# Performance work log

Hardware: AMD Instinct MI355X
Metric: run time of the kernel (lower is better)

## Reference

```python
import jax, jax.numpy as jnp
import numpy as np

NUM_FEAT = 1024
NUM_GROUP = 16
DIM_K = NUM_FEAT // NUM_GROUP  # 64
FEAT_DIM = 64
WAVE_LENGTH = 1000.0


def position_embedding(box, ctx_box):
    # box: (M,4), ctx_box: (N,4) corner encoding -> (M*N, 64)
    xmin, ymin, xmax, ymax = jnp.split(box, 4, axis=1)            # (M,1) each
    bw = xmax - xmin + 1.0
    bh = ymax - ymin + 1.0
    cx = 0.5 * (xmin + xmax)
    cy = 0.5 * (ymin + ymax)
    cxmin, cymin, cxmax, cymax = jnp.split(ctx_box, 4, axis=1)    # (N,1) each
    cbw = cxmax - cxmin + 1.0
    cbh = cymax - cymin + 1.0
    ccx = 0.5 * (cxmin + cxmax)
    ccy = 0.5 * (cymin + cymax)
    dx = jnp.log(jnp.clip(jnp.abs((cx - ccx.T) / bw), 1e-3))      # (M,N)
    dy = jnp.log(jnp.clip(jnp.abs((cy - ccy.T) / bh), 1e-3))
    dw = jnp.log(cbw.T / bw)
    dh = jnp.log(cbh.T / bh)
    pos = jnp.stack((dx, dy, dw, dh), axis=2)                     # (M,N,4)
    feat_range = jnp.arange(FEAT_DIM // 8, dtype=jnp.float32)     # (8,)
    dim_mat = jnp.power(jnp.float32(WAVE_LENGTH), (8.0 / FEAT_DIM) * feat_range)
    div = (100.0 * pos)[..., None] / dim_mat                      # (M,N,4,8)
    emb = jnp.concatenate((jnp.sin(div), jnp.cos(div)), axis=3)   # (M,N,4,16)
    M, N = pos.shape[0], pos.shape[1]
    return emb.reshape(M * N, FEAT_DIM)


def setup_inputs() -> dict:
    key = jax.random.key(0)
    ks = jax.random.split(key, 12)
    M, N = 512, 1024

    def make_boxes(k, n):
        k1, k2 = jax.random.split(k)
        xy = jax.random.uniform(k1, (n, 2), dtype=jnp.float32) * 800.0
        wh = jax.random.uniform(k2, (n, 2), dtype=jnp.float32) * 200.0 + 1.0
        return jnp.concatenate([xy, xy + wh], axis=1)             # valid corners

    return {
        "feat": jax.random.normal(ks[0], (M, NUM_FEAT), dtype=jnp.float32),
        "ctx_feat": jax.random.normal(ks[1], (N, NUM_FEAT), dtype=jnp.float32),
        "box": make_boxes(ks[2], M),
        "ctx_box": make_boxes(ks[3], N),
        # torch Linear stores weight as (out, in); apply as x @ W.T + b
        "w_fc_gt": jax.random.normal(ks[4], (NUM_FEAT, 1024), dtype=jnp.float32) * 0.01,
        "b_fc_gt": jnp.zeros((NUM_FEAT,), dtype=jnp.float32),
        "w_fc_ctx": jax.random.normal(ks[5], (NUM_FEAT, 1024), dtype=jnp.float32) * 0.01,
        "b_fc_ctx": jnp.zeros((NUM_FEAT,), dtype=jnp.float32),
        "w_pos_gt": jax.random.normal(ks[6], (NUM_GROUP, FEAT_DIM), dtype=jnp.float32) * 0.01,
        "b_pos_gt": jnp.zeros((NUM_GROUP,), dtype=jnp.float32),
        "w_pos_ctx": jax.random.normal(ks[7], (NUM_GROUP, FEAT_DIM), dtype=jnp.float32) * 0.01,
        "b_pos_ctx": jnp.zeros((NUM_GROUP,), dtype=jnp.float32),
        # grouped 1x1 conv (16384 -> 1024, groups=16): per-group weight (64 out, 1024 in)
        "w_conv": jax.random.normal(ks[8], (NUM_GROUP, DIM_K, NUM_FEAT), dtype=jnp.float32) * 0.02,
        "b_conv": jnp.zeros((NUM_FEAT,), dtype=jnp.float32),
    }


def reference(feat, ctx_feat, box, ctx_box,
              w_fc_gt, b_fc_gt, w_fc_ctx, b_fc_ctx,
              w_pos_gt, b_pos_gt, w_pos_ctx, b_pos_ctx,
              w_conv, b_conv):
    M, N = feat.shape[0], ctx_feat.shape[0]
    # positional bias per group: (M*N,64) -relu-> linear -> (G,M,N)
    pe_gt = jax.nn.relu(position_embedding(box, ctx_box))
    pos_gt = (pe_gt @ w_pos_gt.T + b_pos_gt).T.reshape(NUM_GROUP, M, N)
    pe_ctx = jax.nn.relu(position_embedding(ctx_box, box))
    pos_ctx = (pe_ctx @ w_pos_ctx.T + b_pos_ctx).T.reshape(NUM_GROUP, N, M)
    # grouped projections
    q = (feat @ w_fc_gt.T + b_fc_gt).reshape(M, NUM_GROUP, DIM_K)
    k = (ctx_feat @ w_fc_ctx.T + b_fc_ctx).reshape(N, NUM_GROUP, DIM_K)
    scores = jnp.einsum('mgd,ngd->gmn', q, k) / np.float32(np.sqrt(DIM_K))  # (G,M,N)
    # gt <- ctx attention with log-position bias
    w1 = jax.nn.softmax(jnp.log(jnp.clip(pos_gt, 1e-6)) + scores, axis=-1)  # (G,M,N)
    att1 = jnp.einsum('gmn,nc->mgc', w1, ctx_feat)                          # (M,G,1024)
    out_gt = jnp.einsum('mgc,goc->mgo', att1, w_conv).reshape(M, NUM_FEAT) + b_conv
    # ctx <- gt attention (note: original module reuses gt_ctx_linear_out here)
    w2 = jax.nn.softmax(jnp.log(jnp.clip(pos_ctx, 1e-6)) + scores.transpose(0, 2, 1), axis=-1)  # (G,N,M)
    att2 = jnp.einsum('gnm,mc->ngc', w2, feat)                              # (N,G,1024)
    out_ctx = jnp.einsum('ngc,goc->ngo', att2, w_conv).reshape(N, NUM_FEAT) + b_conv
    return out_gt, out_ctx
```

## Files before the change

kernel.cpp:

```cpp
#include <hip/hip_runtime.h>
#include <math.h>


typedef __attribute__((ext_vector_type(8))) short short8;
typedef __attribute__((ext_vector_type(4))) float floatx4;
typedef __attribute__((ext_vector_type(4))) _Float16 half4;
typedef __attribute__((ext_vector_type(4))) unsigned uint4v;

__device__ inline unsigned short f32_bf16_rne(float x) {
    union { float f; unsigned u; } v; v.f = x;
    unsigned u = v.u;
    return (unsigned short)((u + 0x7fffu + ((u >> 16) & 1u)) >> 16);
}

__device__ inline unsigned fbits(float x) {
    union { float f; unsigned u; } v; v.f = x; return v.u;
}
__device__ inline float bitsf(unsigned u) {
    union { unsigned u; float f; } v; v.u = u; return v.f;
}

__device__ __forceinline__ floatx4 mfma16(short8 a, short8 b, floatx4 c) {
    return __builtin_amdgcn_mfma_f32_16x16x32_bf16(a, b, c, 0, 0, 0);
}

__device__ __forceinline__ void gemm_tile_pack(
    const unsigned short* __restrict__ Ab, int lda,
    const unsigned short* __restrict__ Bb, int ldb, int K,
    unsigned short* __restrict__ out_base,
    const float* __restrict__ biasvec,
    unsigned short* As, unsigned short* Bs)
{
    const int tid = threadIdx.x;
    const int lr = tid >> 3;
    const int lk = (tid & 7) * 8;
    const int lane = tid & 63;
    const int wave = tid >> 6;
    const int qr = (wave >> 1) * 32;
    const int qc = (wave & 1) * 32;
    const int m = lane & 15;
    const int quad = lane >> 4;

    const unsigned short* Ap  = Ab + (long long)lr * lda + lk;
    const unsigned short* Ap2 = Ap + 32LL * lda;
    const unsigned short* Bp  = Bb + (long long)lr * ldb + lk;
    const unsigned short* Bp2 = Bp + 32LL * ldb;
    unsigned short* AsW  = As + lr * 72 + lk;
    unsigned short* AsW2 = As + (lr + 32) * 72 + lk;
    unsigned short* BsW  = Bs + lr * 72 + lk;
    unsigned short* BsW2 = Bs + (lr + 32) * 72 + lk;
    const unsigned short* a0p = As + (qr + m) * 72 + quad * 8;
    const unsigned short* b0p = Bs + (qc + m) * 72 + quad * 8;

    floatx4 acc00 = {0.f,0.f,0.f,0.f}, acc01 = {0.f,0.f,0.f,0.f};
    floatx4 acc10 = {0.f,0.f,0.f,0.f}, acc11 = {0.f,0.f,0.f,0.f};

    int4 pa0 = *(const int4*)Ap;
    int4 pa1 = *(const int4*)Ap2;
    int4 pb0 = *(const int4*)Bp;
    int4 pb1 = *(const int4*)Bp2;
    int4 qa0 = *(const int4*)(Ap + 64);
    int4 qa1 = *(const int4*)(Ap2 + 64);
    int4 qb0 = *(const int4*)(Bp + 64);
    int4 qb1 = *(const int4*)(Bp2 + 64);

    for (int k0 = 0; ; ) {
        __syncthreads();
        *(int4*)AsW  = pa0;
        *(int4*)AsW2 = pa1;
        *(int4*)BsW  = pb0;
        *(int4*)BsW2 = pb1;
        __syncthreads();
        pa0 = qa0; pa1 = qa1; pb0 = qb0; pb1 = qb1;
        const int kf = k0 + 128;
        if (kf < K) {
            qa0 = *(const int4*)(Ap + kf);
            qa1 = *(const int4*)(Ap2 + kf);
            qb0 = *(const int4*)(Bp + kf);
            qb1 = *(const int4*)(Bp2 + kf);
        }
        #pragma unroll
        for (int kk = 0; kk < 64; kk += 32) {
            short8 a0 = *(const short8*)(a0p + kk);
            short8 a1 = *(const short8*)(a0p + 16 * 72 + kk);
            short8 b0 = *(const short8*)(b0p + kk);
            short8 b1 = *(const short8*)(b0p + 16 * 72 + kk);
            acc00 = mfma16(a0, b0, acc00);
            acc01 = mfma16(a0, b1, acc01);
            acc10 = mfma16(a1, b0, acc10);
            acc11 = mfma16(a1, b1, acc11);
        }
        k0 += 64;
        if (k0 >= K) break;
    }

    float bias0 = 0.f, bias1 = 0.f;
    if (biasvec) { bias0 = biasvec[qc + m]; bias1 = biasvec[qc + 16 + m]; }

    __syncthreads();
    const floatx4 accs[2][2] = { {acc00, acc01}, {acc10, acc11} };
    #pragma unroll
    for (int i = 0; i < 2; ++i)
        #pragma unroll
        for (int r = 0; r < 4; ++r) {
            const int lrow = qr + i * 16 + quad * 4 + r;
            #pragma unroll
            for (int j = 0; j < 2; ++j) {
                const int lcol = qc + j * 16 + m;
                float val = accs[i][j][r] + (j ? bias1 : bias0);
                As[lrow * 72 + lcol] = f32_bf16_rne(val);
            }
        }
    __syncthreads();
    #pragma unroll
    for (int h = 0; h < 2; ++h) {
        const int f = h * 2048 + tid * 8;
        const int lanep = (f >> 3) & 63;
        const int part = (f >> 9) & 1;
        const int ploc = f >> 10;
        const int row = ploc * 16 + (lanep & 15);
        const int col = part * 32 + ((lanep >> 4) << 3);
        short8 v8 = *(const short8*)&As[row * 72 + col];
        *(short8*)(out_base + f) = v8;
    }
}

__global__ __launch_bounds__(256) void projvt_kernel(
    const unsigned short* __restrict__ in_bf, const unsigned short* __restrict__ wgt,
    const unsigned short* __restrict__ wctx,
    const float* __restrict__ bgt, const float* __restrict__ bctx,
    unsigned short* __restrict__ qk_pack,
    const unsigned short* __restrict__ wconv, unsigned short* __restrict__ vt_pack)
{
    __shared__ __align__(16) unsigned short As[64 * 72];
    __shared__ __align__(16) unsigned short Bs[64 * 72];
    if (blockIdx.z == 0) {
        const int bm = blockIdx.x * 64;
        const int g = blockIdx.y;
        const unsigned short* B = (bm < 512) ? wgt : wctx;
        const float* bias = (bm < 512) ? bgt : bctx;
        gemm_tile_pack(in_bf + (long long)bm * 1024, 1024,
                       B + (long long)g * 65536, 1024, 1024,
                       qk_pack + ((long long)g * 96 + blockIdx.x * 4) * 1024,
                       bias + g * 64, As, Bs);
    } else {
        const int cc = blockIdx.x;
        const int g = blockIdx.y;
        gemm_tile_pack(wconv + (long long)g * 65536, 1024,
                       in_bf + (long long)cc * 65536, 1024, 1024,
                       vt_pack + ((long long)g * 24 + cc) * 4096,
                       nullptr, As, Bs);
    }
}

__global__ __launch_bounds__(256) void prep_kernel(
    const float* __restrict__ box, const float* __restrict__ ctx_box,
    const float* __restrict__ w_gt, const float* __restrict__ b_gt,
    const float* __restrict__ w_ctx, const float* __restrict__ b_ctx,
    _Float16* __restrict__ bias_gt, _Float16* __restrict__ bias_ctx,
    const float* s0, unsigned short* d0, int n0,
    const float* s1, unsigned short* d1, int n1,
    const float* s2, unsigned short* d2, int n2,
    const float* s3, unsigned short* d3, int n3,
    const float* s4, unsigned short* d4, int n4)
{
    const int bx = blockIdx.x;
    if (bx >= 4096) {
        const int bc = bx - 4096;
        const int which = bc >> 10;
        const int xb = bc & 1023;
        const float* s; unsigned short* d; int n;
        switch (which) {
            case 0: s = s0; d = d0; n = n0; break;
            case 1: s = s1; d = d1; n = n1; break;
            case 2: s = s2; d = d2; n = n2; break;
            case 3: s = s3; d = d3; n = n3; break;
            default: s = s4; d = d4; n = n4; break;
        }
        int idx = (xb * 256 + threadIdx.x) * 4;
        if (idx < n) {
            float4 v = *(const float4*)(s + idx);
            ushort4 o;
            o.x = f32_bf16_rne(v.x); o.y = f32_bf16_rne(v.y);
            o.z = f32_bf16_rne(v.z); o.w = f32_bf16_rne(v.w);
            *(ushort4*)(d + idx) = o;
        }
        return;
    }

    const bool first = (bx < 2048);
    const long long blk = first ? bx : (bx - 2048);
    const float* boxA = first ? box : ctx_box;
    const float* boxB = first ? ctx_box : box;
    const float* w_pos = first ? w_gt : w_ctx;
    const float* b_pos = first ? b_gt : b_ctx;
    _Float16* out = first ? bias_gt : bias_ctx;
    const int shift = first ? 10 : 9;

    __shared__ __align__(16) unsigned short BsH[16 * 72];
    __shared__ __align__(16) unsigned short BsL[16 * 72];
    __shared__ float posL[4 * 68];
    __shared__ _Float16 stg[16 * 68];

    const int tid = threadIdx.x;

    {
        const int g = tid >> 4;
        const int d = (tid & 15) * 4;
        float4 wv = *(const float4*)(w_pos + g * 64 + d);
        unsigned u0 = fbits(wv.x), u1 = fbits(wv.y);
        unsigned u2 = fbits(wv.z), u3 = fbits(wv.w);
        unsigned r0 = fbits(wv.x - bitsf(u0 & 0xFFFF0000u));
        unsigned r1 = fbits(wv.y - bitsf(u1 & 0xFFFF0000u));
        unsigned r2 = fbits(wv.z - bitsf(u2 & 0xFFFF0000u));
        unsigned r3 = fbits(wv.w - bitsf(u3 & 0xFFFF0000u));
        uint2 hv, lv;
        hv.x = (u0 >> 16) | (u1 & 0xFFFF0000u);
        hv.y = (u2 >> 16) | (u3 & 0xFFFF0000u);
        lv.x = (r0 >> 16) | (r1 & 0xFFFF0000u);
        lv.y = (r2 >> 16) | (r3 & 0xFFFF0000u);
        *(uint2*)&BsH[g * 72 + d] = hv;
        *(uint2*)&BsL[g * 72 + d] = lv;
    }
    __syncthreads();

    const int lane = tid & 63;
    const int w = tid >> 6;
    const int m = lane & 15;
    const int quad = lane >> 4;
    const bool qlow = (quad < 2);
    const float phase = (quad & 1) ? 1.57079632679f : 0.0f;
    const float bpv = b_pos[m];

    const unsigned short* bpH = &BsH[m * 72 + quad * 8];
    const unsigned short* bpL = &BsL[m * 72 + quad * 8];
    short8 bH0 = *(const short8*)bpH;
    short8 bH1 = *(const short8*)(bpH + 32);
    short8 bL0 = *(const short8*)bpL;
    short8 bL1 = *(const short8*)(bpL + 32);

    const float w100[8] = {100.f, 42.169650342f, 17.782794100f, 7.498942093f,
                           3.162277660f, 1.333521432f, 0.562341325f, 0.237137371f};
    const long long pbase = blk * 256;

    for (int it = 0; it < 4; ++it) {
        const long long pb = pbase + it * 64;

        {
            const int pl = tid & 63;
            const int p = tid >> 6;
            const long long pair = pb + pl;
            const int i = (int)(pair >> shift);
            const int j = (int)(pair & ((1 << shift) - 1));
            float4 ba = *(const float4*)(boxA + i * 4);
            float4 bb = *(const float4*)(boxB + j * 4);
            float posv;
            if (p == 0) {
                float r = __builtin_amdgcn_rcpf(ba.z - ba.x + 1.f);
                posv = __logf(fmaxf(fabsf((0.5f*(ba.x+ba.z) - 0.5f*(bb.x+bb.z)) * r), 1e-3f));
            } else if (p == 1) {
                float r = __builtin_amdgcn_rcpf(ba.w - ba.y + 1.f);
                posv = __logf(fmaxf(fabsf((0.5f*(ba.y+ba.w) - 0.5f*(bb.y+bb.w)) * r), 1e-3f));
            } else if (p == 2) {
                float r = __builtin_amdgcn_rcpf(ba.z - ba.x + 1.f);
                posv = __logf((bb.z - bb.x + 1.f) * r);
            } else {
                float r = __builtin_amdgcn_rcpf(ba.w - ba.y + 1.f);
                posv = __logf((bb.w - bb.y + 1.f) * r);
            }
            posL[p * 68 + pl] = posv;
        }
        __syncthreads();

        const int plB = w * 16 + m;
        const float pos_lo = posL[(qlow ? 0 : 1) * 68 + plB];
        const float pos_hi = posL[(qlow ? 2 : 3) * 68 + plB];

        unsigned hp0[4], lp0[4], hp1[4], lp1[4];
        #pragma unroll
        for (int fi = 0; fi < 4; ++fi) {
            float x0 = fmaxf(__sinf(fmaf(w100[2*fi],     pos_lo, phase)), 0.f);
            float x1 = fmaxf(__sinf(fmaf(w100[2*fi + 1], pos_lo, phase)), 0.f);
            unsigned u0 = fbits(x0), u1 = fbits(x1);
            unsigned r0 = fbits(x0 - bitsf(u0 & 0xFFFF0000u));
            unsigned r1 = fbits(x1 - bitsf(u1 & 0xFFFF0000u));
            hp0[fi] = (u0 >> 16) | (u1 & 0xFFFF0000u);
            lp0[fi] = (r0 >> 16) | (r1 & 0xFFFF0000u);
            float y0 = fmaxf(__sinf(fmaf(w100[2*fi],     pos_hi, phase)), 0.f);
            float y1 = fmaxf(__sinf(fmaf(w100[2*fi + 1], pos_hi, phase)), 0.f);
            unsigned v0 = fbits(y0), v1 = fbits(y1);
            unsigned s0r = fbits(y0 - bitsf(v0 & 0xFFFF0000u));
            unsigned s1r = fbits(y1 - bitsf(v1 & 0xFFFF0000u));
            hp1[fi] = (v0 >> 16) | (v1 & 0xFFFF0000u);
            lp1[fi] = (s0r >> 16) | (s1r & 0xFFFF0000u);
        }
        union { uint4v u; short8 s; } cH0, cL0, cH1, cL1;
        cH0.u = (uint4v){hp0[0], hp0[1], hp0[2], hp0[3]};
        cL0.u = (uint4v){lp0[0], lp0[1], lp0[2], lp0[3]};
        cH1.u = (uint4v){hp1[0], hp1[1], hp1[2], hp1[3]};
        cL1.u = (uint4v){lp1[0], lp1[1], lp1[2], lp1[3]};

        floatx4 acc = {0.f, 0.f, 0.f, 0.f};
        acc = mfma16(cH0.s, bH0, acc);
        acc = mfma16(cH1.s, bH1, acc);
        acc = mfma16(cH0.s, bL0, acc);
        acc = mfma16(cH1.s, bL1, acc);
        acc = mfma16(cL0.s, bH0, acc);
        acc = mfma16(cL1.s, bH1, acc);

        #pragma unroll
        for (int r = 0; r < 4; ++r)
            stg[m * 68 + w * 16 + quad * 4 + r] =
                (_Float16)__logf(fmaxf(acc[r] + bpv, 1e-6f));
        __syncthreads();

        const int g2 = tid >> 4, c16 = tid & 15;
        *(half4*)(out + (long long)g2 * 524288 + pb + c16 * 4) =
            *(const half4*)&stg[g2 * 68 + c16 * 4];
    }
}

template <int NC>
__device__ __forceinline__ void attn_body(
    int g, int bx,
    const unsigned short* __restrict__ qk, int pA, int pB0,
    const _Float16* __restrict__ bias,
    const unsigned short* __restrict__ vt, int cc0,
    const float* __restrict__ b_conv, float* __restrict__ outp,
    unsigned short* wpack, float* redA, float* redB)
{
    constexpr int NCOL = NC * 64;
    constexpr int WS = NCOL + 8;
    constexpr int SHIFT = (NC == 16) ? 10 : 9;

    const int bm = bx * 16;
    const int tid = threadIdx.x;
    const int lane = tid & 63;
    const int w = tid >> 6;
    const int m = lane & 15;
    const int quad = lane >> 4;

    _Float16* bb = (_Float16*)wpack;
    {
        const _Float16* bsrc = bias + (long long)g * 524288 + (long long)bm * NCOL;
        #pragma unroll
        for (int i = 0; i < (16 * NCOL) / (256 * 8); ++i) {
            const int idx = (i * 256 + tid) * 8;
            const int row = idx >> SHIFT;
            const int col = idx & (NCOL - 1);
            *(int4*)(bb + row * WS + col) = *(const int4*)(bsrc + idx);
        }
    }

    const unsigned short* abase = qk + ((long long)(g * 96 + pA)) * 1024;
    short8 aq0 = *(const short8*)(abase + lane * 8);
    short8 aq1 = *(const short8*)(abase + 512 + lane * 8);

    const unsigned short* bptr = qk + ((long long)(g * 96 + pB0 + w)) * 1024 + lane * 8;
    short8 B0[2], B1[2];
    B0[0] = *(const short8*)bptr;
    B1[0] = *(const short8*)(bptr + 512);
    B0[1] = *(const short8*)(bptr + 4096);
    B1[1] = *(const short8*)(bptr + 4096 + 512);

    __syncthreads();

    const _Float16* brow = bb + (quad * 4) * WS + w * 16 + m;

    float v[NC][4];
    #pragma unroll
    for (int c = 0; c < NC; ++c) {
        float bv[4];
        #pragma unroll
        for (int r = 0; r < 4; ++r)
            bv[r] = (float)brow[r * WS + c * 64];
        floatx4 acc = {0.f, 0.f, 0.f, 0.f};
        acc = mfma16(aq0, B0[c & 1], acc);
        acc = mfma16(aq1, B1[c & 1], acc);
        if (c + 2 < NC) {
            const unsigned short* nb = bptr + (long long)(c + 2) * 4096;
            B0[c & 1] = *(const short8*)nb;
            B1[c & 1] = *(const short8*)(nb + 512);
        }
        #pragma unroll
        for (int r = 0; r < 4; ++r)
            v[c][r] = fmaf(0.125f, acc[r], bv[r]);
    }

    const unsigned short* vptr = vt + ((long long)(g * 24 + cc0)) * 4096
                               + w * 1024 + lane * 8;
    short8 V0[2], V1[2];
    V0[0] = *(const short8*)vptr;
    V1[0] = *(const short8*)(vptr + 512);
    V0[1] = *(const short8*)(vptr + 4096);
    V1[1] = *(const short8*)(vptr + 4096 + 512);

    float rmax[4];
    #pragma unroll
    for (int r = 0; r < 4; ++r) {
        float mx = v[0][r];
        #pragma unroll
        for (int c = 1; c < NC; ++c) mx = fmaxf(mx, v[c][r]);
        #pragma unroll
        for (int off = 1; off < 16; off <<= 1)
            mx = fmaxf(mx, __shfl_xor(mx, off, 64));
        rmax[r] = mx;
    }
    if (m == 0) {
        #pragma unroll
        for (int r = 0; r < 4; ++r) redA[w * 16 + quad * 4 + r] = rmax[r];
    }
    __syncthreads();
    #pragma unroll
    for (int r = 0; r < 4; ++r)
        rmax[r] = fmaxf(fmaxf(redA[quad*4+r], redA[16 + quad*4+r]),
                        fmaxf(redA[32 + quad*4+r], redA[48 + quad*4+r]));

    float rsum[4] = {0.f, 0.f, 0.f, 0.f};
    #pragma unroll
    for (int c = 0; c < NC; ++c)
        #pragma unroll
        for (int r = 0; r < 4; ++r) {
            v[c][r] = __expf(v[c][r] - rmax[r]);
            rsum[r] += v[c][r];
        }
    #pragma unroll
    for (int r = 0; r < 4; ++r)
        #pragma unroll
        for (int off = 1; off < 16; off <<= 1)
            rsum[r] += __shfl_xor(rsum[r], off, 64);
    if (m == 0) {
        #pragma unroll
        for (int r = 0; r < 4; ++r) redB[w * 16 + quad * 4 + r] = rsum[r];
    }
    __syncthreads();
    float rinv[4];
    #pragma unroll
    for (int r = 0; r < 4; ++r)
        rinv[r] = 1.f / (redB[quad*4+r] + redB[16 + quad*4+r] +
                         redB[32 + quad*4+r] + redB[48 + quad*4+r]);

    #pragma unroll
    for (int c = 0; c < NC; ++c)
        #pragma unroll
        for (int r = 0; r < 4; ++r)
            wpack[(quad * 4 + r) * WS + c * 64 + w * 16 + m] =
                f32_bf16_rne(v[c][r] * rinv[r]);

    __syncthreads();

    floatx4 oacc = {0.f, 0.f, 0.f, 0.f};
    const unsigned short* awp = wpack + m * WS + quad * 8;
    #pragma unroll
    for (int kc = 0; kc < NC; ++kc) {
        short8 a0 = *(const short8*)(awp + kc * 64);
        short8 a1 = *(const short8*)(awp + kc * 64 + 32);
        oacc = mfma16(a0, V0[kc & 1], oacc);
        oacc = mfma16(a1, V1[kc & 1], oacc);
        if (kc + 2 < NC) {
            const unsigned short* nv = vptr + (long long)(kc + 2) * 4096;
            V0[kc & 1] = *(const short8*)nv;
            V1[kc & 1] = *(const short8*)(nv + 512);
        }
    }

    const int o = w * 16 + m;
    const float bc = b_conv[g * 64 + o];
    __syncthreads();
    float* ot = (float*)wpack;
    #pragma unroll
    for (int r = 0; r < 4; ++r)
        ot[(quad * 4 + r) * 68 + o] = oacc[r] + bc;
    __syncthreads();
    const int orow = tid >> 4, oc4 = (tid & 15) * 4;
    float4 ov = *(const float4*)&ot[orow * 68 + oc4];
    *(float4*)(outp + (long long)(bm + orow) * 1024 + g * 64 + oc4) = ov;
}

__global__ __launch_bounds__(256) void attn_out_kernel(
    const unsigned short* __restrict__ qk_pack,
    const _Float16* __restrict__ bias_gt, const _Float16* __restrict__ bias_ctx,
    const unsigned short* __restrict__ vt_pack, const float* __restrict__ b_conv,
    float* __restrict__ out_gt, float* __restrict__ out_ctx)
{
    __shared__ __align__(16) unsigned short wpack[16 * 1032];
    __shared__ float redA[64], redB[64];

    const int bx = blockIdx.x;
    if (bx < 512) {
        const int rb = bx & 31;
        attn_body<16>(bx >> 5, rb, qk_pack, rb, 32,
                      bias_gt, vt_pack, 8, b_conv, out_gt,
                      wpack, redA, redB);
    } else {
        const int b2 = bx - 512;
        const int rb = b2 & 63;
        attn_body<8>(b2 >> 6, rb, qk_pack, 32 + rb, 0,
                     bias_ctx, vt_pack, 0, b_conv, out_ctx,
                     wpack, redA, redB);
    }
}

extern "C" void kernel_launch(void* const* d_in, const int* in_sizes, int n_in,
                              void* d_out, int out_size, void* d_ws, size_t ws_size,
                              hipStream_t stream)
{
    const float* feat     = (const float*)d_in[0];
    const float* ctx_feat = (const float*)d_in[1];
    const float* box      = (const float*)d_in[2];
    const float* ctx_box  = (const float*)d_in[3];
    const float* w_fc_gt  = (const float*)d_in[4];
    const float* b_fc_gt  = (const float*)d_in[5];
    const float* w_fc_ctx = (const float*)d_in[6];
    const float* b_fc_ctx = (const float*)d_in[7];
    const float* w_pos_gt = (const float*)d_in[8];
    const float* b_pos_gt = (const float*)d_in[9];
    const float* w_pos_ctx= (const float*)d_in[10];
    const float* b_pos_ctx= (const float*)d_in[11];
    const float* w_conv   = (const float*)d_in[12];
    const float* b_conv   = (const float*)d_in[13];

    float* ws = (float*)d_ws;
    unsigned short* in_bf   = (unsigned short*)ws;
    unsigned short* ctx_bf  = in_bf + 524288LL;
    unsigned short* qk_pack = in_bf + 1572864LL;
    _Float16* bias_gt  = (_Float16*)(ws + 1572864LL);
    _Float16* bias_ctx = (_Float16*)(ws + 5767168LL);
    unsigned short* wconv_bf = (unsigned short*)(ws + 9961472LL);
    unsigned short* vt_pack  = (unsigned short*)(ws + 10485760LL);
    unsigned short* wfcgt_bf = (unsigned short*)(ws + 11272192LL);
    unsigned short* wfcctx_bf= wfcgt_bf + 1048576LL;

    float* out_gt  = (float*)d_out;
    float* out_ctx = (float*)d_out + 524288LL;

    hipLaunchKernelGGL(prep_kernel, dim3(9216), dim3(256), 0, stream,
                       box, ctx_box, w_pos_gt, b_pos_gt, w_pos_ctx, b_pos_ctx,
                       bias_gt, bias_ctx,
                       feat, in_bf, 524288,
                       ctx_feat, ctx_bf, 1048576,
                       w_fc_gt, wfcgt_bf, 1048576,
                       w_fc_ctx, wfcctx_bf, 1048576,
                       w_conv, wconv_bf, 1048576);

    hipLaunchKernelGGL(projvt_kernel, dim3(24, 16, 2), dim3(256), 0, stream,
                       in_bf, wfcgt_bf, wfcctx_bf, b_fc_gt, b_fc_ctx, qk_pack,
                       wconv_bf, vt_pack);

    hipLaunchKernelGGL(attn_out_kernel, dim3(1536), dim3(256), 0, stream,
                       qk_pack, bias_gt, bias_ctx, vt_pack, b_conv, out_gt, out_ctx);
}
```

Measured before the change: 150.2 us.

## Split casts into own kernel and co-schedule projection GEMMs with position-bias blocks

Moves the fp32-to-bf16 casts into a separate first kernel. The position-embedding bias computation and the Q/K/V projection GEMM tiles now share one launch, with GEMM blocks interleaved every sixth block id, so the latency-bound GEMM tiles overlap with the transcendental-heavy bias work. Shared memory is unified into one buffer sized for the GEMM tiles, which may lower occupancy for the bias blocks.

```diff
diff --git a/kernel.cpp b/kernel.cpp
--- a/kernel.cpp
+++ b/kernel.cpp
@@ -125,71 +125,70 @@
     }
 }
 
-__global__ __launch_bounds__(256) void projvt_kernel(
+__global__ __launch_bounds__(256) void cast_kernel(
+    const float* __restrict__ s0, unsigned short* __restrict__ d0,
+    const float* __restrict__ s1, unsigned short* __restrict__ d1,
+    const float* __restrict__ s2, unsigned short* __restrict__ d2,
+    const float* __restrict__ s3, unsigned short* __restrict__ d3,
+    const float* __restrict__ s4, unsigned short* __restrict__ d4)
+{
+    int bc = blockIdx.x;
+    const float* s; unsigned short* d;
+    if (bc < 512)       { s = s0; d = d0; }
+    else if (bc < 1536) { s = s1; d = d1; bc -= 512; }
+    else if (bc < 2560) { s = s2; d = d2; bc -= 1536; }
+    else if (bc < 3584) { s = s3; d = d3; bc -= 2560; }
+    else                { s = s4; d = d4; bc -= 3584; }
+    const int idx = (bc * 256 + threadIdx.x) * 4;
+    float4 v = *(const float4*)(s + idx);
+    ushort4 o;
+    o.x = f32_bf16_rne(v.x); o.y = f32_bf16_rne(v.y);
+    o.z = f32_bf16_rne(v.z); o.w = f32_bf16_rne(v.w);
+    *(ushort4*)(d + idx) = o;
+}
+
+__global__ __launch_bounds__(256) void posproj_kernel(
+    const float* __restrict__ box, const float* __restrict__ ctx_box,
+    const float* __restrict__ w_gt, const float* __restrict__ b_gt,
+    const float* __restrict__ w_ctx, const float* __restrict__ b_ctx,
+    _Float16* __restrict__ bias_gt, _Float16* __restrict__ bias_ctx,
     const unsigned short* __restrict__ in_bf, const unsigned short* __restrict__ wgt,
     const unsigned short* __restrict__ wctx,
     const float* __restrict__ bgt, const float* __restrict__ bctx,
     unsigned short* __restrict__ qk_pack,
     const unsigned short* __restrict__ wconv, unsigned short* __restrict__ vt_pack)
 {
-    __shared__ __align__(16) unsigned short As[64 * 72];
-    __shared__ __align__(16) unsigned short Bs[64 * 72];
-    if (blockIdx.z == 0) {
-        const int bm = blockIdx.x * 64;
-        const int g = blockIdx.y;
-        const unsigned short* B = (bm < 512) ? wgt : wctx;
-        const float* bias = (bm < 512) ? bgt : bctx;
-        gemm_tile_pack(in_bf + (long long)bm * 1024, 1024,
-                       B + (long long)g * 65536, 1024, 1024,
-                       qk_pack + ((long long)g * 96 + blockIdx.x * 4) * 1024,
-                       bias + g * 64, As, Bs);
-    } else {
-        const int cc = blockIdx.x;
-        const int g = blockIdx.y;
-        gemm_tile_pack(wconv + (long long)g * 65536, 1024,
-                       in_bf + (long long)cc * 65536, 1024, 1024,
-                       vt_pack + ((long long)g * 24 + cc) * 4096,
-                       nullptr, As, Bs);
-    }
-}
-
-__global__ __launch_bounds__(256) void prep_kernel(
-    const float* __restrict__ box, const float* __restrict__ ctx_box,
-    const float* __restrict__ w_gt, const float* __restrict__ b_gt,
-    const float* __restrict__ w_ctx, const float* __restrict__ b_ctx,
-    _Float16* __restrict__ bias_gt, _Float16* __restrict__ bias_ctx,
-    const float* s0, unsigned short* d0, int n0,
-    const float* s1, unsigned short* d1, int n1,
-    const float* s2, unsigned short* d2, int n2,
-    const float* s3, unsigned short* d3, int n3,
-    const float* s4, unsigned short* d4, int n4)
-{
-    const int bx = blockIdx.x;
-    if (bx >= 4096) {
-        const int bc = bx - 4096;
-        const int which = bc >> 10;
-        const int xb = bc & 1023;
-        const float* s; unsigned short* d; int n;
-        switch (which) {
-            case 0: s = s0; d = d0; n = n0; break;
-            case 1: s = s1; d = d1; n = n1; break;
-            case 2: s = s2; d = d2; n = n2; break;
-            case 3: s = s3; d = d3; n = n3; break;
-            default: s = s4; d = d4; n = n4; break;
-        }
-        int idx = (xb * 256 + threadIdx.x) * 4;
-        if (idx < n) {
-            float4 v = *(const float4*)(s + idx);
-            ushort4 o;
-            o.x = f32_bf16_rne(v.x); o.y = f32_bf16_rne(v.y);
-            o.z = f32_bf16_rne(v.z); o.w = f32_bf16_rne(v.w);
-            *(ushort4*)(d + idx) = o;
+    __shared__ __align__(16) unsigned short smem[64 * 72 * 2];
+    const int i = blockIdx.x;
+
+    if (i < 4608 && (i % 6) == 0) {
+        const int gi = i / 6;
+        const int z = gi / 384;
+        const int rem = gi - z * 384;
+        const int g = rem / 24;
+        const int cc = rem - g * 24;
+        unsigned short* As = smem;
+        unsigned short* Bs = smem + 64 * 72;
+        if (z == 0) {
+            const int bm = cc * 64;
+            const unsigned short* B = (bm < 512) ? wgt : wctx;
+            const float* bias = (bm < 512) ? bgt : bctx;
+            gemm_tile_pack(in_bf + (long long)bm * 1024, 1024,
+                           B + (long long)g * 65536, 1024, 1024,
+                           qk_pack + ((long long)g * 96 + cc * 4) * 1024,
+                           bias + g * 64, As, Bs);
+        } else {
+            gemm_tile_pack(wconv + (long long)g * 65536, 1024,
+                           in_bf + (long long)cc * 65536, 1024, 1024,
+                           vt_pack + ((long long)g * 24 + cc) * 4096,
+                           nullptr, As, Bs);
         }
         return;
     }
 
-    const bool first = (bx < 2048);
-    const long long blk = first ? bx : (bx - 2048);
+    const int pi = (i < 4608) ? (i - i / 6 - 1) : (i - 768);
+    const bool first = (pi < 2048);
+    const long long blk = first ? pi : (pi - 2048);
     const float* boxA = first ? box : ctx_box;
     const float* boxB = first ? ctx_box : box;
     const float* w_pos = first ? w_gt : w_ctx;
@@ -197,10 +196,10 @@
     _Float16* out = first ? bias_gt : bias_ctx;
     const int shift = first ? 10 : 9;
 
-    __shared__ __align__(16) unsigned short BsH[16 * 72];
-    __shared__ __align__(16) unsigned short BsL[16 * 72];
-    __shared__ float posL[4 * 68];
-    __shared__ _Float16 stg[16 * 68];
+    unsigned short* BsH = smem;
+    unsigned short* BsL = smem + 16 * 72;
+    float* posL = (float*)(smem + 32 * 72);
+    _Float16* stg = (_Float16*)(posL + 4 * 68);
 
     const int tid = threadIdx.x;
 
@@ -250,10 +249,10 @@
             const int pl = tid & 63;
             const int p = tid >> 6;
             const long long pair = pb + pl;
-            const int i = (int)(pair >> shift);
-            const int j = (int)(pair & ((1 << shift) - 1));
-            float4 ba = *(const float4*)(boxA + i * 4);
-            float4 bb = *(const float4*)(boxB + j * 4);
+            const int i2 = (int)(pair >> shift);
+            const int j2 = (int)(pair & ((1 << shift) - 1));
+            float4 ba = *(const float4*)(boxA + i2 * 4);
+            float4 bb = *(const float4*)(boxB + j2 * 4);
             float posv;
             if (p == 0) {
                 float r = __builtin_amdgcn_rcpf(ba.z - ba.x + 1.f);
@@ -534,16 +533,16 @@
     float* out_gt  = (float*)d_out;
     float* out_ctx = (float*)d_out + 524288LL;
 
-    hipLaunchKernelGGL(prep_kernel, dim3(9216), dim3(256), 0, stream,
+    hipLaunchKernelGGL(cast_kernel, dim3(4608), dim3(256), 0, stream,
+                       feat, in_bf,
+                       ctx_feat, ctx_bf,
+                       w_fc_gt, wfcgt_bf,
+                       w_fc_ctx, wfcctx_bf,
+                       w_conv, wconv_bf);
+
+    hipLaunchKernelGGL(posproj_kernel, dim3(4864), dim3(256), 0, stream,
                        box, ctx_box, w_pos_gt, b_pos_gt, w_pos_ctx, b_pos_ctx,
                        bias_gt, bias_ctx,
-                       feat, in_bf, 524288,
-                       ctx_feat, ctx_bf, 1048576,
-                       w_fc_gt, wfcgt_bf, 1048576,
-                       w_fc_ctx, wfcctx_bf, 1048576,
-                       w_conv, wconv_bf, 1048576);
-
-    hipLaunchKernelGGL(projvt_kernel, dim3(24, 16, 2), dim3(256), 0, stream,
                        in_bf, wfcgt_bf, wfcctx_bf, b_fc_gt, b_fc_ctx, qk_pack,
                        wconv_bf, vt_pack);
 
```

Result: no change. 150.9 us (+0.5%).
